# Kernel optimization log

Measured on AMD Instinct MI355X. Metric: run time of the kernel, lower is better.

The kernel has to match this reference:

```python
import jax, jax.numpy as jnp
import numpy as np

B, H, DH = 1, 16, 128
HID, MLP = 2048, 8192
LT, LI = 256, 2048
L = LT + LI


def _layernorm(x, eps=1e-6):
    mu = jnp.mean(x, axis=-1, keepdims=True)
    var = jnp.mean((x - mu) ** 2, axis=-1, keepdims=True)
    return (x - mu) * jax.lax.rsqrt(var + eps)


def _rmsnorm(x, scale, eps=1e-6):
    rr = jax.lax.rsqrt(jnp.mean(x * x, axis=-1, keepdims=True) + eps)
    return x * rr * scale


def _apply_rope(x, pe):
    # x: (B,H,L,D) -> (B,H,L,D/2,1,2); pe: (B,1,L,D/2,2,2)
    xs = x.reshape(*x.shape[:-1], -1, 1, 2)
    out = pe[..., 0] * xs[..., 0] + pe[..., 1] * xs[..., 1]  # (B,H,L,D/2,2)
    return out.reshape(x.shape)


def _qkv_split(x, w, b):
    Bv, Lv, _ = x.shape
    qkv = (x @ w + b).reshape(Bv, Lv, 3, H, DH).transpose(2, 0, 3, 1, 4)  # K B H L D
    return qkv[0], qkv[1], qkv[2]


def setup_inputs() -> dict:
    key = jax.random.key(0)
    ks = jax.random.split(key, 16)
    s = 0.02
    inp = {
        'img': jax.random.normal(ks[0], (B, LI, HID), jnp.float32),
        'txt': jax.random.normal(ks[1], (B, LT, HID), jnp.float32),
        'vec': jax.random.normal(ks[2], (B, HID), jnp.float32),
        'img_mod_w': s * jax.random.normal(ks[3], (HID, 6 * HID), jnp.float32),
        'img_mod_b': jnp.zeros((6 * HID,), jnp.float32),
        'txt_mod_w': s * jax.random.normal(ks[4], (HID, 6 * HID), jnp.float32),
        'txt_mod_b': jnp.zeros((6 * HID,), jnp.float32),
        'img_qkv_w': s * jax.random.normal(ks[5], (HID, 3 * HID), jnp.float32),
        'img_qkv_b': jnp.zeros((3 * HID,), jnp.float32),
        'img_q_scale': jnp.ones((DH,), jnp.float32),
        'img_k_scale': jnp.ones((DH,), jnp.float32),
        'txt_qkv_w': s * jax.random.normal(ks[6], (HID, 3 * HID), jnp.float32),
        'txt_qkv_b': jnp.zeros((3 * HID,), jnp.float32),
        'txt_q_scale': jnp.ones((DH,), jnp.float32),
        'txt_k_scale': jnp.ones((DH,), jnp.float32),
        'img_proj_w': s * jax.random.normal(ks[7], (HID, HID), jnp.float32),
        'img_proj_b': jnp.zeros((HID,), jnp.float32),
        'txt_proj_w': s * jax.random.normal(ks[8], (HID, HID), jnp.float32),
        'txt_proj_b': jnp.zeros((HID,), jnp.float32),
        'img_mlp_w1': s * jax.random.normal(ks[9], (HID, MLP), jnp.float32),
        'img_mlp_b1': jnp.zeros((MLP,), jnp.float32),
        'img_mlp_w2': s * jax.random.normal(ks[10], (MLP, HID), jnp.float32),
        'img_mlp_b2': jnp.zeros((HID,), jnp.float32),
        'txt_mlp_w1': s * jax.random.normal(ks[11], (HID, MLP), jnp.float32),
        'txt_mlp_b1': jnp.zeros((MLP,), jnp.float32),
        'txt_mlp_w2': s * jax.random.normal(ks[12], (MLP, HID), jnp.float32),
        'txt_mlp_b2': jnp.zeros((HID,), jnp.float32),
    }
    # Real RoPE rotation matrices [[cos,-sin],[sin,cos]]: (1,1,L,DH/2,2,2)
    pos = jnp.arange(L, dtype=jnp.float32)
    freqs = 1.0 / (10000.0 ** (jnp.arange(DH // 2, dtype=jnp.float32) / (DH // 2)))
    ang = pos[:, None] * freqs[None, :]
    c, sn = jnp.cos(ang), jnp.sin(ang)
    pe = jnp.stack([jnp.stack([c, -sn], -1), jnp.stack([sn, c], -1)], -2)  # (L,DH/2,2,2)
    inp['pe'] = pe[None, None]
    return inp


def reference(img, txt, vec, pe,
              img_mod_w, img_mod_b, txt_mod_w, txt_mod_b,
              img_qkv_w, img_qkv_b, img_q_scale, img_k_scale,
              txt_qkv_w, txt_qkv_b, txt_q_scale, txt_k_scale,
              img_proj_w, img_proj_b, txt_proj_w, txt_proj_b,
              img_mlp_w1, img_mlp_b1, img_mlp_w2, img_mlp_b2,
              txt_mlp_w1, txt_mlp_b1, txt_mlp_w2, txt_mlp_b2):
    # AdaLN modulation: SiLU(vec) @ W -> 6 chunks of (B,1,HID)
    im = jnp.split(jax.nn.silu(vec) @ img_mod_w + img_mod_b, 6, axis=-1)
    i_sh1, i_sc1, i_g1, i_sh2, i_sc2, i_g2 = [m[:, None, :] for m in im]
    tm = jnp.split(jax.nn.silu(vec) @ txt_mod_w + txt_mod_b, 6, axis=-1)
    t_sh1, t_sc1, t_g1, t_sh2, t_sc2, t_g2 = [m[:, None, :] for m in tm]

    img_mod = (1 + i_sc1) * _layernorm(img) + i_sh1
    iq, ik, iv = _qkv_split(img_mod, img_qkv_w, img_qkv_b)
    iq = _rmsnorm(iq, img_q_scale)
    ik = _rmsnorm(ik, img_k_scale)

    txt_mod = (1 + t_sc1) * _layernorm(txt) + t_sh1
    tq, tk, tv = _qkv_split(txt_mod, txt_qkv_w, txt_qkv_b)
    tq = _rmsnorm(tq, txt_q_scale)
    tk = _rmsnorm(tk, txt_k_scale)

    # concat text then image along sequence (B,H,L,D)
    q = jnp.concatenate([tq, iq], axis=2)
    k = jnp.concatenate([tk, ik], axis=2)
    v = jnp.concatenate([tv, iv], axis=2)
    q = _apply_rope(q, pe)
    k = _apply_rope(k, pe)

    scores = jnp.einsum('bhqd,bhkd->bhqk', q, k) / np.float32(np.sqrt(DH))
    a = jax.nn.softmax(scores, axis=-1)
    o = jnp.einsum('bhqk,bhkd->bhqd', a, v)
    attn = o.transpose(0, 2, 1, 3).reshape(o.shape[0], -1, H * DH)  # (B,L,HID)

    txt_a, img_a = attn[:, :LT], attn[:, LT:]

    img = img + i_g1 * (img_a @ img_proj_w + img_proj_b)
    h = (1 + i_sc2) * _layernorm(img) + i_sh2
    h = jax.nn.gelu(h @ img_mlp_w1 + img_mlp_b1, approximate=True)
    img = img + i_g2 * (h @ img_mlp_w2 + img_mlp_b2)

    txt = txt + t_g1 * (txt_a @ txt_proj_w + txt_proj_b)
    h = (1 + t_sc2) * _layernorm(txt) + t_sh2
    h = jax.nn.gelu(h @ txt_mlp_w1 + txt_mlp_b1, approximate=True)
    txt = txt + t_g2 * (h @ txt_mlp_w2 + txt_mlp_b2)

    return img, txt
```

## Files before the change

kernel.cpp:

```cpp
#include <hip/hip_runtime.h>

using u16 = unsigned short;
typedef __bf16 bf16x8 __attribute__((ext_vector_type(8)));
typedef float f32x4 __attribute__((ext_vector_type(4)));

__device__ inline u16 f2bf(float f){
  unsigned u = __float_as_uint(f);
  u += 0x7fff + ((u >> 16) & 1);
  return (u16)(u >> 16);
}
__device__ inline float bf2f(u16 u){ return __uint_as_float((unsigned)u << 16); }

__device__ inline float wredsum(float v){
  #pragma unroll
  for (int o = 32; o; o >>= 1) v += __shfl_xor(v, o, 64);
  return v;
}

__device__ inline void gld16(const u16* g, u16* lds){
  __builtin_amdgcn_global_load_lds(
      (const __attribute__((address_space(1))) unsigned int*)g,
      (__attribute__((address_space(3))) unsigned int*)lds, 16, 0, 0);
}

__global__ void mod_mv_k(const float* __restrict__ vec,
    const float* __restrict__ wi, const float* __restrict__ wt,
    float* __restrict__ part)
{
  __shared__ float sv[512];
  __shared__ float red[4][64];
  int tid = threadIdx.x;
  int z = blockIdx.y;
  int k0 = z * 512;
  for (int i = tid; i < 512; i += 256){ float v = vec[k0 + i]; sv[i] = v / (1.0f + __expf(-v)); }
  __syncthreads();
  int j0 = blockIdx.x * 64;
  bool ist = j0 >= 12288;
  const float* w = ist ? wt : wi;
  int col = (ist ? j0 - 12288 : j0) + (tid & 63);
  int kq = tid >> 6;
  float acc = 0.f;
  const float* wp = w + (long long)k0 * 12288 + col;
  for (int k = kq * 128; k < kq * 128 + 128; ++k) acc += sv[k] * wp[(long long)k * 12288];
  red[kq][tid & 63] = acc;
  __syncthreads();
  if (kq == 0)
    part[(long long)z * 24576 + j0 + tid] = red[0][tid] + red[1][tid] + red[2][tid] + red[3][tid];
}

__global__ void mod_comb_k(const float* __restrict__ part,
    const float* __restrict__ bi, const float* __restrict__ bt,
    float* __restrict__ oi, float* __restrict__ ot)
{
  int idx = blockIdx.x * 256 + threadIdx.x;
  float s = part[idx] + part[24576 + idx] + part[2 * 24576 + idx] + part[3 * 24576 + idx];
  if (idx >= 12288) ot[idx - 12288] = s + bt[idx - 12288];
  else              oi[idx] = s + bi[idx];
}

struct TcArgs {
  const float* in[8];
  u16* out[8];
  int K[8];
  int N[8];
  int base[9];
};

__global__ void tcast64_k(TcArgs a)
{
  __shared__ float tile[64][65];
  int bid = blockIdx.x;
  int w = 0;
  #pragma unroll
  for (int i = 0; i < 8; ++i) if (bid >= a.base[i + 1]) w = i + 1;
  const float* in = a.in[w];
  u16* out = a.out[w];
  int K = a.K[w], N = a.N[w];
  int local = bid - a.base[w];
  int tx = N >> 6;
  int n0 = (local % tx) * 64, k0 = (local / tx) * 64;
  int tid = threadIdx.x;
  int r = tid >> 2, c0 = (tid & 3) * 16;
  const float* ir = &in[(long long)(k0 + r) * N + n0 + c0];
  #pragma unroll
  for (int j = 0; j < 4; ++j){
    float4 v = *(const float4*)&ir[j * 4];
    tile[r][c0 + j * 4 + 0] = v.x; tile[r][c0 + j * 4 + 1] = v.y;
    tile[r][c0 + j * 4 + 2] = v.z; tile[r][c0 + j * 4 + 3] = v.w;
  }
  __syncthreads();
  int n = tid >> 2, ks = (tid & 3) * 16;
  u16* orow = &out[(long long)(n0 + n) * K + k0 + ks];
  #pragma unroll
  for (int j = 0; j < 4; ++j){
    ushort4 o;
    o.x = f2bf(tile[ks + j * 4 + 0][n]);
    o.y = f2bf(tile[ks + j * 4 + 1][n]);
    o.z = f2bf(tile[ks + j * 4 + 2][n]);
    o.w = f2bf(tile[ks + j * 4 + 3][n]);
    *(ushort4*)&orow[j * 4] = o;
  }
}

__global__ void ln_mod_k(const float* __restrict__ xi, const float* __restrict__ xt,
    const float* __restrict__ sh_i, const float* __restrict__ sc_i,
    const float* __restrict__ sh_t, const float* __restrict__ sc_t,
    u16* __restrict__ oi, u16* __restrict__ ot)
{
  int row = blockIdx.x, tid = threadIdx.x;
  bool ist = row >= 2048;
  int r = ist ? row - 2048 : row;
  const float* xr = (ist ? xt : xi) + (long long)r * 2048;
  const float* sh = ist ? sh_t : sh_i;
  const float* sc = ist ? sc_t : sc_i;
  u16* orow = (ist ? ot : oi) + (long long)r * 2048;
  float v[8]; float s = 0.f, s2 = 0.f;
  #pragma unroll
  for (int j = 0; j < 8; ++j){ v[j] = xr[tid + j * 256]; s += v[j]; s2 += v[j] * v[j]; }
  s = wredsum(s); s2 = wredsum(s2);
  __shared__ float red[4][2];
  int wave = tid >> 6, lane = tid & 63;
  if (lane == 0){ red[wave][0] = s; red[wave][1] = s2; }
  __syncthreads();
  float S1 = red[0][0] + red[1][0] + red[2][0] + red[3][0];
  float S2 = red[0][1] + red[1][1] + red[2][1] + red[3][1];
  float mu = S1 * (1.0f / 2048.0f);
  float var = S2 * (1.0f / 2048.0f) - mu * mu;
  float rs = rsqrtf(var + 1e-6f);
  #pragma unroll
  for (int j = 0; j < 8; ++j){
    int c = tid + j * 256;
    orow[c] = f2bf((1.0f + sc[c]) * (v[j] - mu) * rs + sh[c]);
  }
}

__global__ __launch_bounds__(512)
void fattn_k(const u16* __restrict__ Qb, const u16* __restrict__ Kb,
             const u16* __restrict__ Vt, u16* __restrict__ attn)
{
  __shared__ u16 Kl[2][64 * 128];
  __shared__ u16 Vl[2][128 * 64];
  __shared__ u16 Pl[128 * 64];

  const int tid  = threadIdx.x;
  const int lane = tid & 63;
  const int wave = tid >> 6;
  const int h  = blockIdx.y;
  const int q0 = blockIdx.x * 128;

  const u16* Qg = Qb + ((long long)h * 2304 + q0) * 128;
  const u16* Kg = Kb + (long long)h * 2304 * 128;
  const u16* Vg = Vt + (long long)h * 128 * 2304;

  u16* Qlds = &Kl[0][0];

  const int r16 = wave * 4 + (lane >> 4);
  const int o16 = lane & 15;
  const int r8 = wave * 8 + (lane >> 3);
  const int o8 = lane & 7;

  #pragma unroll
  for (int i = 0; i < 4; ++i){
    int row = i * 32 + r16;
    gld16(Qg + (long long)row * 128 + ((o16 ^ (row & 7)) * 8),
          Qlds + (i * 32 + wave * 4) * 128);
  }
  __syncthreads();

  const int frow = lane & 15;
  const int j0   = lane >> 4;
  const int qrow = wave * 16 + frow;
  bf16x8 aq[4];
  #pragma unroll
  for (int s = 0; s < 4; ++s)
    aq[s] = *(const bf16x8*)&Qlds[qrow * 128 + (((s * 4 + j0) ^ (qrow & 7)) * 8)];
  __syncthreads();

  auto stageK = [&](int t, int b){
    #pragma unroll
    for (int i = 0; i < 2; ++i){
      int row = i * 32 + r16;
      gld16(Kg + (long long)(t * 64 + row) * 128 + ((o16 ^ (row & 7)) * 8),
            &Kl[b][(i * 32 + wave * 4) * 128]);
    }
  };
  auto stageV = [&](int t, int b){
    #pragma unroll
    for (int i = 0; i < 2; ++i){
      int row = i * 64 + r8;
      gld16(Vg + (long long)row * 2304 + t * 64 + ((o8 ^ (row & 7)) * 8),
            &Vl[b][(i * 64 + wave * 8) * 64]);
    }
  };

  stageK(0, 0); stageV(0, 0);
  __builtin_amdgcn_sched_barrier(0);

  float mrun[4], lrun[4];
  #pragma unroll
  for (int j = 0; j < 4; ++j){ mrun[j] = -3.0e38f; lrun[j] = 0.f; }
  f32x4 oacc[8] = {};

  for (int t = 0; t < 36; ++t){
    const int cur = t & 1;
    asm volatile("s_waitcnt vmcnt(0)" ::: "memory");
    __builtin_amdgcn_sched_barrier(0);
    __builtin_amdgcn_s_barrier();
    __builtin_amdgcn_sched_barrier(0);
    if (t + 1 < 36){ stageK(t + 1, cur ^ 1); stageV(t + 1, cur ^ 1); }
    __builtin_amdgcn_sched_barrier(0);

    f32x4 sacc[4] = {};
    #pragma unroll
    for (int s = 0; s < 4; ++s){
      #pragma unroll
      for (int n = 0; n < 4; ++n){
        int kr = n * 16 + frow;
        bf16x8 bk = *(const bf16x8*)&Kl[cur][kr * 128 + (((s * 4 + j0) ^ (kr & 7)) * 8)];
        sacc[n] = __builtin_amdgcn_mfma_f32_16x16x32_bf16(aq[s], bk, sacc[n], 0, 0, 0);
      }
    }

    float mnew[4], scl[4];
    #pragma unroll
    for (int j = 0; j < 4; ++j){
      float v = fmaxf(fmaxf(sacc[0][j], sacc[1][j]), fmaxf(sacc[2][j], sacc[3][j]));
      #pragma unroll
      for (int o = 8; o; o >>= 1) v = fmaxf(v, __shfl_xor(v, o, 64));
      mnew[j] = fmaxf(mrun[j], v);
      scl[j] = __expf(mrun[j] - mnew[j]);
      mrun[j] = mnew[j];
    }
    #pragma unroll
    for (int j = 0; j < 4; ++j){
      const int row = wave * 16 + j0 * 4 + j;
      float rsum = 0.f;
      #pragma unroll
      for (int n = 0; n < 4; ++n){
        float p = __expf(sacc[n][j] - mnew[j]);
        rsum += p;
        int col = n * 16 + frow;
        Pl[row * 64 + (((col >> 3) ^ (row & 7)) << 3) + (col & 7)] = f2bf(p);
      }
      #pragma unroll
      for (int o = 8; o; o >>= 1) rsum += __shfl_xor(rsum, o, 64);
      lrun[j] = lrun[j] * scl[j] + rsum;
      #pragma unroll
      for (int n = 0; n < 8; ++n) oacc[n][j] *= scl[j];
    }
    asm volatile("s_waitcnt lgkmcnt(0)" ::: "memory");
    __builtin_amdgcn_sched_barrier(0);

    #pragma unroll
    for (int s = 0; s < 2; ++s){
      bf16x8 ap = *(const bf16x8*)&Pl[qrow * 64 + (((s * 4 + j0) ^ (qrow & 7)) * 8)];
      #pragma unroll
      for (int n = 0; n < 8; ++n){
        int dr = n * 16 + frow;
        bf16x8 bv = *(const bf16x8*)&Vl[cur][dr * 64 + (((s * 4 + j0) ^ (dr & 7)) * 8)];
        oacc[n] = __builtin_amdgcn_mfma_f32_16x16x32_bf16(ap, bv, oacc[n], 0, 0, 0);
      }
    }
    __builtin_amdgcn_sched_barrier(0);
  }

  float inv[4];
  #pragma unroll
  for (int j = 0; j < 4; ++j) inv[j] = 1.0f / lrun[j];
  #pragma unroll
  for (int n = 0; n < 8; ++n){
    int d = n * 16 + frow;
    #pragma unroll
    for (int j = 0; j < 4; ++j){
      int row = wave * 16 + j0 * 4 + j;
      attn[(long long)(q0 + row) * 2048 + h * 128 + d] = f2bf(oacc[n][j] * inv[j]);
    }
  }
}

template<int MODE>
__global__ __launch_bounds__(512)
void gemm8_k(const u16* __restrict__ Ai, const u16* __restrict__ At, int lda,
             const u16* __restrict__ Bi, const u16* __restrict__ Bt, int ldb,
             const float* __restrict__ bias_i, const float* __restrict__ bias_t,
             const float* __restrict__ res_i,  const float* __restrict__ res_t,
             const float* __restrict__ gate_i, const float* __restrict__ gate_t,
             void* __restrict__ Ci, void* __restrict__ Ct, int ldc, int K,
             const float* __restrict__ qs_i, const float* __restrict__ ks_i,
             const float* __restrict__ qs_t, const float* __restrict__ ks_t,
             const float* __restrict__ pe,
             u16* __restrict__ Qo, u16* __restrict__ Ko, u16* __restrict__ Vo)
{
  constexpr int BK = 64;
  constexpr int MR = 4, NR = 2;
  constexpr int AI = 2, BI = 2;

  __shared__ u16 As[2][128 * BK];
  __shared__ u16 Bs[2][128 * BK];

  const int tid  = threadIdx.x;
  const int lane = tid & 63;
  const int wave = tid >> 6;
  const int wm = wave >> 2;
  const int wn = wave & 3;

  const int gx = gridDim.x;
  const int nwg = gx * gridDim.y;
  const int n = blockIdx.x + gx * blockIdx.y;
  const int s_id = (n & 7) * (nwg >> 3) + (n >> 3);
  const int bx = s_id % gx;
  const int by = s_id / gx;

  const bool ist = bx >= 16;
  const int rb = ist ? bx - 16 : bx;
  const u16* Ab = (ist ? At : Ai) + (long long)rb * 128 * lda;
  const u16* Bb = (ist ? Bt : Bi) + (long long)by * 128 * ldb;
  const float* bias = ist ? bias_t : bias_i;
  const float* res  = ist ? res_t  : res_i;
  const float* gate = ist ? gate_t : gate_i;
  void* C = ist ? Ct : Ci;

  const int srow = wave * 8 + (lane >> 3);
  const int sgo  = ((lane & 7) ^ ((lane >> 3) & 7)) * 8;
  const u16* agp[AI]; const u16* bgp[BI];
  int alo[AI], blo[BI];
  #pragma unroll
  for (int i = 0; i < AI; ++i){
    agp[i] = Ab + (long long)(i * 64 + srow) * lda + sgo;
    alo[i] = (i * 64 + wave * 8) * BK;
  }
  #pragma unroll
  for (int i = 0; i < BI; ++i){
    bgp[i] = Bb + (long long)(i * 64 + srow) * ldb + sgo;
    blo[i] = (i * 64 + wave * 8) * BK;
  }

  const int arow0 = wm * 64;
  const int frow  = lane & 15;
  const int fx    = lane & 7;
  const int j0    = lane >> 4;

  f32x4 acc[MR][NR] = {};

  #pragma unroll
  for (int i = 0; i < AI; ++i) gld16(agp[i], &As[0][alo[i]]);
  #pragma unroll
  for (int i = 0; i < BI; ++i) gld16(bgp[i], &Bs[0][blo[i]]);
  __builtin_amdgcn_sched_barrier(0);

  const int nt = K / BK;
  for (int t = 0; t < nt; ++t){
    if (t + 1 < nt){
      int k0 = (t + 1) * BK;
      int nb = (t + 1) & 1;
      #pragma unroll
      for (int i = 0; i < AI; ++i) gld16(agp[i] + k0, &As[nb][alo[i]]);
      #pragma unroll
      for (int i = 0; i < BI; ++i) gld16(bgp[i] + k0, &Bs[nb][blo[i]]);
      __builtin_amdgcn_sched_barrier(0);
      asm volatile("s_waitcnt vmcnt(4)" ::: "memory");
    } else {
      asm volatile("s_waitcnt vmcnt(0)" ::: "memory");
    }
    __builtin_amdgcn_sched_barrier(0);
    __builtin_amdgcn_s_barrier();
    __builtin_amdgcn_sched_barrier(0);

    const u16* as = As[t & 1];
    const u16* bs = Bs[t & 1];
    #pragma unroll
    for (int s = 0; s < 2; ++s){
      const int oct = (s * 4 + j0) ^ fx;
      bf16x8 bfr[NR];
      #pragma unroll
      for (int nn = 0; nn < NR; ++nn)
        bfr[nn] = *(const bf16x8*)&bs[(wn * 32 + nn * 16 + frow) * BK + oct * 8];
      __builtin_amdgcn_s_setprio(1);
      #pragma unroll
      for (int m = 0; m < MR; ++m){
        bf16x8 af = *(const bf16x8*)&as[(arow0 + m * 16 + frow) * BK + oct * 8];
        #pragma unroll
        for (int nn = 0; nn < NR; ++nn)
          acc[m][nn] = __builtin_amdgcn_mfma_f32_16x16x32_bf16(af, bfr[nn], acc[m][nn], 0, 0, 0);
      }
      __builtin_amdgcn_s_setprio(0);
    }
    __builtin_amdgcn_sched_barrier(0);
    __builtin_amdgcn_s_barrier();
    __builtin_amdgcn_sched_barrier(0);
  }

  const int lr = (lane >> 4) * 4;
  const int lc = lane & 15;

  if constexpr (MODE == 4){
    const int sstr = by >> 4;
    const int hh = by & 15;
    const int d0 = wn * 32;
    const long long posb = (ist ? 0 : 256) + (long long)rb * 128;
    float* red = (float*)&As[0][0];
    #pragma unroll
    for (int mi = 0; mi < MR; ++mi)
      #pragma unroll
      for (int ni = 0; ni < NR; ++ni){
        float bv = bias[by * 128 + d0 + ni * 16 + lc];
        #pragma unroll
        for (int j = 0; j < 4; ++j) acc[mi][ni][j] += bv;
      }
    if (sstr < 2){
      #pragma unroll
      for (int mi = 0; mi < MR; ++mi)
        #pragma unroll
        for (int j = 0; j < 4; ++j){
          float p = acc[mi][0][j] * acc[mi][0][j] + acc[mi][1][j] * acc[mi][1][j];
          #pragma unroll
          for (int o = 1; o < 16; o <<= 1) p += __shfl_xor(p, o, 64);
          if (lc == 0) red[(arow0 + mi * 16 + lr + j) * 4 + wn] = p;
        }
      __syncthreads();
      const float* scale = (sstr == 0) ? (ist ? qs_t : qs_i) : (ist ? ks_t : ks_i);
      const float fold = (sstr == 0) ? 0.08838834764831845f : 1.0f;
      u16* Out = (sstr == 0) ? Qo : Ko;
      #pragma unroll
      for (int mi = 0; mi < MR; ++mi)
        #pragma unroll
        for (int j = 0; j < 4; ++j){
          int rl = arow0 + mi * 16 + lr + j;
          float tot = red[rl * 4 + 0] + red[rl * 4 + 1] + red[rl * 4 + 2] + red[rl * 4 + 3];
          float rr = rsqrtf(tot * (1.0f / 128.0f) + 1e-6f) * fold;
          long long pos = posb + rl;
          u16* orow = Out + ((long long)hh * 2304 + pos) * 128;
          #pragma unroll
          for (int ni = 0; ni < NR; ++ni){
            int d = d0 + ni * 16 + lc;
            float xn = acc[mi][ni][j] * rr * scale[d];
            float pr = __shfl_xor(xn, 1, 64);
            int aa = d & 1;
            const float* pp = pe + pos * 256 + (d >> 1) * 4 + aa * 2;
            float e  = aa ? pr : xn;
            float o_ = aa ? xn : pr;
            orow[d] = f2bf(pp[0] * e + pp[1] * o_);
          }
        }
    } else {
      #pragma unroll
      for (int mi = 0; mi < MR; ++mi){
        long long pb = posb + arow0 + mi * 16 + lr;
        #pragma unroll
        for (int ni = 0; ni < NR; ++ni){
          int d = d0 + ni * 16 + lc;
          ushort4 o4;
          o4.x = f2bf(acc[mi][ni][0]); o4.y = f2bf(acc[mi][ni][1]);
          o4.z = f2bf(acc[mi][ni][2]); o4.w = f2bf(acc[mi][ni][3]);
          *(ushort4*)&Vo[((long long)hh * 128 + d) * 2304 + pb] = o4;
        }
      }
    }
    return;
  }

  const long long rowb = (long long)rb * 128 + arow0;
  const long long colb = (long long)by * 128 + wn * 32;
  #pragma unroll
  for (int mi = 0; mi < MR; ++mi){
    #pragma unroll
    for (int ni = 0; ni < NR; ++ni){
      long long col = colb + ni * 16 + lc;
      float bv = bias ? bias[col] : 0.0f;
      #pragma unroll
      for (int j = 0; j < 4; ++j){
        long long row = rowb + mi * 16 + lr + j;
        float v = acc[mi][ni][j] + bv;
        long long ci = row * (long long)ldc + col;
        if constexpr (MODE == 0) ((float*)C)[ci] = v;
        else if constexpr (MODE == 2) ((float*)C)[ci] = res[ci] + gate[col] * v;
        else {
          float z2 = 1.5957691216057308f * (v + 0.044715f * v * v * v);
          ((u16*)C)[ci] = f2bf(v / (1.0f + __expf(-z2)));
        }
      }
    }
  }
}

extern "C" void kernel_launch(void* const* d_in, const int* in_sizes, int n_in,
                              void* d_out, int out_size, void* d_ws, size_t ws_size,
                              hipStream_t stream)
{
  const float* img        = (const float*)d_in[0];
  const float* txt        = (const float*)d_in[1];
  const float* vec        = (const float*)d_in[2];
  const float* img_mod_w  = (const float*)d_in[3];
  const float* img_mod_b  = (const float*)d_in[4];
  const float* txt_mod_w  = (const float*)d_in[5];
  const float* txt_mod_b  = (const float*)d_in[6];
  const float* img_qkv_w  = (const float*)d_in[7];
  const float* img_qkv_b  = (const float*)d_in[8];
  const float* img_q_s    = (const float*)d_in[9];
  const float* img_k_s    = (const float*)d_in[10];
  const float* txt_qkv_w  = (const float*)d_in[11];
  const float* txt_qkv_b  = (const float*)d_in[12];
  const float* txt_q_s    = (const float*)d_in[13];
  const float* txt_k_s    = (const float*)d_in[14];
  const float* img_proj_w = (const float*)d_in[15];
  const float* img_proj_b = (const float*)d_in[16];
  const float* txt_proj_w = (const float*)d_in[17];
  const float* txt_proj_b = (const float*)d_in[18];
  const float* img_mlp_w1 = (const float*)d_in[19];
  const float* img_mlp_b1 = (const float*)d_in[20];
  const float* img_mlp_w2 = (const float*)d_in[21];
  const float* img_mlp_b2 = (const float*)d_in[22];
  const float* txt_mlp_w1 = (const float*)d_in[23];
  const float* txt_mlp_b1 = (const float*)d_in[24];
  const float* txt_mlp_w2 = (const float*)d_in[25];
  const float* txt_mlp_b2 = (const float*)d_in[26];
  const float* pe         = (const float*)d_in[27];

  char* ws = (char*)d_ws;
  size_t off = 0;
  auto alloc = [&](size_t b){ void* p = ws + off; off = (off + b + 255) & ~(size_t)255; return p; };

  u16* wq_i = (u16*)alloc(6144ll * 2048 * 2);
  u16* wq_t = (u16*)alloc(6144ll * 2048 * 2);
  u16* wp_i = (u16*)alloc(2048ll * 2048 * 2);
  u16* wp_t = (u16*)alloc(2048ll * 2048 * 2);
  u16* w1_i = (u16*)alloc(8192ll * 2048 * 2);
  u16* w1_t = (u16*)alloc(8192ll * 2048 * 2);
  u16* w2_i = (u16*)alloc(2048ll * 8192 * 2);
  u16* w2_t = (u16*)alloc(2048ll * 8192 * 2);
  float* mod_i = (float*)alloc(12288 * 4);
  float* mod_t = (float*)alloc(12288 * 4);
  float* mpart = (float*)alloc(4ll * 24576 * 4);
  u16* Qb   = (u16*)alloc(16ll * 2304 * 128 * 2);
  u16* Kb   = (u16*)alloc(16ll * 2304 * 128 * 2);
  u16* Vt   = (u16*)alloc(16ll * 2304 * 128 * 2);
  u16* attn = (u16*)alloc(2304ll * 2048 * 2);
  char* big = (char*)alloc(4ll * 2304 * 2304 * 4);

  u16*   xin_i = (u16*)big;
  u16*   xin_t = (u16*)(big + 8388608);
  float* y1_i  = (float*)big;
  float* y1_t  = (float*)(big + 16777216);
  u16*   ln2_i = (u16*)(big + 18874368);
  u16*   ln2_t = (u16*)(big + 27262976);
  u16*   h_i   = (u16*)(big + 28311552);
  u16*   h_t   = (u16*)(big + 61865984);

  mod_mv_k<<<dim3(384, 4), 256, 0, stream>>>(vec, img_mod_w, txt_mod_w, mpart);
  mod_comb_k<<<96, 256, 0, stream>>>(mpart, img_mod_b, txt_mod_b, mod_i, mod_t);

  {
    TcArgs a;
    const float* ins[8] = {img_qkv_w, txt_qkv_w, img_proj_w, txt_proj_w,
                           img_mlp_w1, txt_mlp_w1, img_mlp_w2, txt_mlp_w2};
    u16* outs[8] = {wq_i, wq_t, wp_i, wp_t, w1_i, w1_t, w2_i, w2_t};
    int Ks[8] = {2048, 2048, 2048, 2048, 2048, 2048, 8192, 8192};
    int Ns[8] = {6144, 6144, 2048, 2048, 8192, 8192, 2048, 2048};
    int b = 0;
    for (int i = 0; i < 8; ++i){
      a.in[i] = ins[i]; a.out[i] = outs[i]; a.K[i] = Ks[i]; a.N[i] = Ns[i];
      a.base[i] = b;
      b += (Ks[i] >> 6) * (Ns[i] >> 6);
    }
    a.base[8] = b;
    tcast64_k<<<b, 256, 0, stream>>>(a);
  }

  ln_mod_k<<<2304, 256, 0, stream>>>(img, txt, mod_i, mod_i + 2048, mod_t, mod_t + 2048, xin_i, xin_t);

  gemm8_k<4><<<dim3(18, 48), 512, 0, stream>>>(xin_i, xin_t, 2048, wq_i, wq_t, 2048,
      img_qkv_b, txt_qkv_b, nullptr, nullptr, nullptr, nullptr, nullptr, nullptr, 0, 2048,
      img_q_s, img_k_s, txt_q_s, txt_k_s, pe, Qb, Kb, Vt);

  fattn_k<<<dim3(18, 16), 512, 0, stream>>>(Qb, Kb, Vt, attn);

  gemm8_k<2><<<dim3(18, 16), 512, 0, stream>>>(attn + 256 * 2048, attn, 2048, wp_i, wp_t, 2048,
      img_proj_b, txt_proj_b, img, txt, mod_i + 4096, mod_t + 4096, y1_i, y1_t, 2048, 2048,
      nullptr, nullptr, nullptr, nullptr, nullptr, nullptr, nullptr, nullptr);

  ln_mod_k<<<2304, 256, 0, stream>>>(y1_i, y1_t, mod_i + 6144, mod_i + 8192, mod_t + 6144, mod_t + 8192, ln2_i, ln2_t);

  gemm8_k<3><<<dim3(18, 64), 512, 0, stream>>>(ln2_i, ln2_t, 2048, w1_i, w1_t, 2048,
      img_mlp_b1, txt_mlp_b1, nullptr, nullptr, nullptr, nullptr, h_i, h_t, 8192, 2048,
      nullptr, nullptr, nullptr, nullptr, nullptr, nullptr, nullptr, nullptr);

  float* out_img = (float*)d_out;
  float* out_txt = out_img + 2048ll * 2048;
  gemm8_k<2><<<dim3(18, 16), 512, 0, stream>>>(h_i, h_t, 8192, w2_i, w2_t, 8192,
      img_mlp_b2, txt_mlp_b2, y1_i, y1_t, mod_i + 10240, mod_t + 10240, out_img, out_txt, 2048, 8192,
      nullptr, nullptr, nullptr, nullptr, nullptr, nullptr, nullptr, nullptr);
}
```

Baseline: 777.8 us.

## Use 256x256-tile pipelined GEMM kernel for MLP up-projection with fused GELU

Adds a dedicated GEMM kernel for the MLP first layer that computes 256x256 output tiles per workgroup as four 128x128 quadrants. The loads of the next K-slice are staged per quadrant and interleaved with MFMA work, separated by barriers and waitcnt. A grid-index remap spreads workgroups across the XCDs. Each loaded tile is reused by more MFMAs, which cuts global and LDS traffic per flop compared with the 128-tile kernel. The cost is 64 KB of LDS, a large accumulator register footprint, and fewer workgroups (288), so occupancy and tail effects may suffer.

```diff
diff --git a/kernel.cpp b/kernel.cpp
--- a/kernel.cpp
+++ b/kernel.cpp
@@ -278,6 +278,147 @@
   }
 }
 
+__global__ __launch_bounds__(512)
+void gemm10_k(const u16* __restrict__ Ai, const u16* __restrict__ At, int lda,
+              const u16* __restrict__ Bi, const u16* __restrict__ Bt, int ldb,
+              const float* __restrict__ bias_i, const float* __restrict__ bias_t,
+              u16* __restrict__ Ci, u16* __restrict__ Ct, int ldc, int K)
+{
+  constexpr int BK = 64;
+  __shared__ u16 Ah[2][2][128 * BK];
+  __shared__ u16 Bh[2][2][128 * BK];
+
+  const int tid  = threadIdx.x;
+  const int lane = tid & 63;
+  const int wave = tid >> 6;
+  const int wm = wave >> 2;
+  const int wn = wave & 3;
+
+  const int gx = gridDim.x;
+  const int nwg = gx * gridDim.y;
+  const int n = blockIdx.x + gx * blockIdx.y;
+  const int s_id = (n & 7) * (nwg >> 3) + (n >> 3);
+  const int bx = s_id % gx;
+  const int by = s_id / gx;
+
+  const bool ist = (bx == 8);
+  const u16* Ab = ist ? At : (Ai + (long long)bx * 256 * lda);
+  const u16* Bb = (ist ? Bt : Bi) + (long long)by * 256 * ldb;
+  const float* bias = ist ? bias_t : bias_i;
+  u16* C = ist ? Ct : Ci;
+
+  const int srow = wave * 8 + (lane >> 3);
+  const int sgo  = ((lane & 7) ^ ((lane >> 3) & 7)) * 8;
+  auto stageA = [&](int h, int b, int kk){
+    #pragma unroll
+    for (int i = 0; i < 2; ++i)
+      gld16(Ab + (long long)(h * 128 + i * 64 + srow) * lda + kk + sgo,
+            &Ah[b][h][(i * 64 + wave * 8) * BK]);
+  };
+  auto stageB = [&](int h, int b, int kk){
+    #pragma unroll
+    for (int i = 0; i < 2; ++i)
+      gld16(Bb + (long long)(h * 128 + i * 64 + srow) * ldb + kk + sgo,
+            &Bh[b][h][(i * 64 + wave * 8) * BK]);
+  };
+
+  const int frow = lane & 15;
+  const int fx   = lane & 7;
+  const int j0   = lane >> 4;
+
+  f32x4 acc[2][4][2][2] = {};
+  bf16x8 afA[2][4], bfA[2][2];
+  bf16x8 afB[2][4], bfB[2][2];
+
+  #define READQ(mh, nh, b, AF, BF)                                                     \
+    _Pragma("unroll")                                                                  \
+    for (int s = 0; s < 2; ++s){                                                       \
+      const int oct = ((s * 4 + j0) ^ fx) * 8;                                         \
+      _Pragma("unroll")                                                                \
+      for (int i = 0; i < 4; ++i)                                                      \
+        AF[s][i] = *(const bf16x8*)&Ah[b][mh][(wm * 64 + i * 16 + frow) * BK + oct];   \
+      _Pragma("unroll")                                                                \
+      for (int k2 = 0; k2 < 2; ++k2)                                                   \
+        BF[s][k2] = *(const bf16x8*)&Bh[b][nh][(wn * 32 + k2 * 16 + frow) * BK + oct]; \
+    }
+
+  #define MFMAQ(mh, nh, AF, BF)                                                        \
+    __builtin_amdgcn_s_setprio(1);                                                     \
+    _Pragma("unroll")                                                                  \
+    for (int s = 0; s < 2; ++s)                                                        \
+      _Pragma("unroll")                                                                \
+      for (int i = 0; i < 4; ++i)                                                      \
+        _Pragma("unroll")                                                              \
+        for (int k2 = 0; k2 < 2; ++k2)                                                 \
+          acc[mh][i][nh][k2] = __builtin_amdgcn_mfma_f32_16x16x32_bf16(                \
+              AF[s][i], BF[s][k2], acc[mh][i][nh][k2], 0, 0, 0);                       \
+    __builtin_amdgcn_s_setprio(0);
+
+  const int nt = K / BK;
+  stageA(0, 0, 0); stageB(0, 0, 0); stageA(1, 0, 0); stageB(1, 0, 0);
+  stageA(0, 1, BK); stageB(0, 1, BK);
+  __builtin_amdgcn_sched_barrier(0);
+
+  for (int t = 0; t < nt; ++t){
+    const int b = t & 1, nb = b ^ 1;
+    if (t + 1 < nt) stageA(1, nb, (t + 1) * BK);
+    __builtin_amdgcn_sched_barrier(0);
+    if (t == nt - 1) asm volatile("s_waitcnt vmcnt(0)" ::: "memory");
+    else             asm volatile("s_waitcnt vmcnt(6)" ::: "memory");
+    __builtin_amdgcn_sched_barrier(0);
+    __builtin_amdgcn_s_barrier();
+    __builtin_amdgcn_sched_barrier(0);
+    READQ(0, 0, b, afA, bfA);
+    MFMAQ(0, 0, afA, bfA);
+    READQ(0, 1, b, afB, bfB);
+    __builtin_amdgcn_sched_barrier(0);
+    __builtin_amdgcn_s_barrier();
+    __builtin_amdgcn_sched_barrier(0);
+    if (t + 1 < nt) stageB(1, nb, (t + 1) * BK);
+    __builtin_amdgcn_sched_barrier(0);
+    MFMAQ(0, 1, afB, bfB);
+    READQ(1, 0, b, afA, bfA);
+    __builtin_amdgcn_sched_barrier(0);
+    __builtin_amdgcn_s_barrier();
+    __builtin_amdgcn_sched_barrier(0);
+    if (t + 2 < nt) stageA(0, b, (t + 2) * BK);
+    __builtin_amdgcn_sched_barrier(0);
+    MFMAQ(1, 0, afA, bfA);
+    READQ(1, 1, b, afB, bfB);
+    __builtin_amdgcn_sched_barrier(0);
+    __builtin_amdgcn_s_barrier();
+    __builtin_amdgcn_sched_barrier(0);
+    if (t + 2 < nt) stageB(0, b, (t + 2) * BK);
+    __builtin_amdgcn_sched_barrier(0);
+    MFMAQ(1, 1, afB, bfB);
+    __builtin_amdgcn_sched_barrier(0);
+    __builtin_amdgcn_s_barrier();
+    __builtin_amdgcn_sched_barrier(0);
+  }
+  #undef READQ
+  #undef MFMAQ
+
+  const long long rowbase = ist ? 0 : (long long)bx * 256;
+  #pragma unroll
+  for (int mh = 0; mh < 2; ++mh)
+    #pragma unroll
+    for (int i = 0; i < 4; ++i)
+      #pragma unroll
+      for (int nh = 0; nh < 2; ++nh)
+        #pragma unroll
+        for (int k2 = 0; k2 < 2; ++k2){
+          long long col = (long long)by * 256 + nh * 128 + wn * 32 + k2 * 16 + frow;
+          float bv = bias[col];
+          #pragma unroll
+          for (int jj = 0; jj < 4; ++jj){
+            long long row = rowbase + mh * 128 + wm * 64 + i * 16 + j0 * 4 + jj;
+            float v = acc[mh][i][nh][k2][jj] + bv;
+            float z2 = 1.5957691216057308f * (v + 0.044715f * v * v * v);
+            C[row * (long long)ldc + col] = f2bf(v / (1.0f + __expf(-z2)));
+          }
+        }
+}
+
 template<int MODE>
 __global__ __launch_bounds__(512)
 void gemm8_k(const u16* __restrict__ Ai, const u16* __restrict__ At, int lda,
@@ -474,10 +615,6 @@
         long long ci = row * (long long)ldc + col;
         if constexpr (MODE == 0) ((float*)C)[ci] = v;
         else if constexpr (MODE == 2) ((float*)C)[ci] = res[ci] + gate[col] * v;
-        else {
-          float z2 = 1.5957691216057308f * (v + 0.044715f * v * v * v);
-          ((u16*)C)[ci] = f2bf(v / (1.0f + __expf(-z2)));
-        }
       }
     }
   }
@@ -580,9 +717,8 @@
 
   ln_mod_k<<<2304, 256, 0, stream>>>(y1_i, y1_t, mod_i + 6144, mod_i + 8192, mod_t + 6144, mod_t + 8192, ln2_i, ln2_t);
 
-  gemm8_k<3><<<dim3(18, 64), 512, 0, stream>>>(ln2_i, ln2_t, 2048, w1_i, w1_t, 2048,
-      img_mlp_b1, txt_mlp_b1, nullptr, nullptr, nullptr, nullptr, h_i, h_t, 8192, 2048,
-      nullptr, nullptr, nullptr, nullptr, nullptr, nullptr, nullptr, nullptr);
+  gemm10_k<<<dim3(9, 32), 512, 0, stream>>>(ln2_i, ln2_t, 2048, w1_i, w1_t, 2048,
+      img_mlp_b1, txt_mlp_b1, h_i, h_t, 8192, 2048);
 
   float* out_img = (float*)d_out;
   float* out_txt = out_img + 2048ll * 2048;
```

Measured after the change: 817.8 us. +5.1%, slower.
